# Kernel tuning notes

Hardware: AMD Instinct MI355X
Metric: run time of the kernel (lower is better)

The kernel has to match this reference:

```python
import jax, jax.numpy as jnp
import numpy as np

B, C, H, W = 16, 64, 64, 64
K_CLUST, KS, OUT, RANK, MLP = 16, 3, 64, 8, 32
F = C * KS * KS  # 576


def setup_inputs() -> dict:
    key = jax.random.key(0)
    ks = jax.random.split(key, 14)
    rn = lambda k, shp, s=0.05: (jax.random.normal(k, shp, jnp.float32) * s)
    return {
        "x": jax.random.normal(ks[0], (B, C, H, W), jnp.float32),
        "labels": jax.random.randint(ks[1], (B, H, W), 0, K_CLUST),
        "lr_w1": rn(ks[2], (F, MLP)), "lr_b1": rn(ks[3], (MLP,)),
        "lr_w2": rn(ks[4], (MLP, MLP)), "lr_b2": rn(ks[5], (MLP,)),
        "lr_w3": rn(ks[6], (MLP, RANK)), "lr_b3": rn(ks[7], (RANK,)),
        "base_kernels": rn(ks[8], (RANK, F, OUT), 0.1),
        "bw1": rn(ks[9], (F, MLP)), "bb1": rn(ks[10], (MLP,)),
        "bw2": rn(ks[11], (MLP, OUT)), "bb2": rn(ks[12], (OUT,)),
    }


def _extract_patches(x):
    # torch nn.Unfold(kernel=3, padding=1) layout: features ordered (C, kh, kw)
    b, c, h, w = x.shape
    xp = jnp.pad(x, ((0, 0), (0, 0), (1, 1), (1, 1)))
    p = jnp.stack([xp[:, :, i:i + h, j:j + w] for i in range(KS) for j in range(KS)], axis=2)  # [B,C,9,H,W]
    return p.reshape(b, c * KS * KS, h * w).transpose(0, 2, 1)  # [B, HW, F]


def reference(x, labels, lr_w1, lr_b1, lr_w2, lr_b2, lr_w3, lr_b3,
              base_kernels, bw1, bb1, bw2, bb2):
    b, c, h, w = x.shape
    patches = _extract_patches(x)                              # [B, HW, F]
    lab = labels.reshape(b, -1)                                # [B, HW]
    onehot = jax.nn.one_hot(lab, K_CLUST, dtype=patches.dtype) # [B, HW, K]
    counts = onehot.sum(axis=1)                                # [B, K]
    centers = jnp.einsum('bnk,bnf->bkf', onehot, patches) / (counts[:, :, None] + 1e-6)

    hdn = jax.nn.relu(centers @ lr_w1 + lr_b1)
    hdn = jax.nn.relu(hdn @ lr_w2 + lr_b2)
    lowrank = hdn @ lr_w3 + lr_b3                              # [B, K, R]
    bias = jax.nn.relu(centers @ bw1 + bb1) @ bw2 + bb2        # [B, K, O]

    kernels = jnp.einsum('bkr,rfo->bkfo', lowrank, base_kernels)   # [B, K, F, O]
    scores = jnp.einsum('bnf,bkfo->bnko', patches, kernels)        # [B, HW, K, O]
    out = jnp.einsum('bnko,bnk->bno', scores, onehot)
    out = out + jnp.einsum('bko,bnk->bno', bias, onehot)           # per-pixel cluster bias
    return out.reshape(b, h, w, OUT).transpose(0, 3, 1, 2)         # [B, O, H, W]
```

## Files before the change

kernel.cpp:

```cpp
#include <hip/hip_runtime.h>
#include <stdint.h>
#include <stddef.h>

#define NB   16
#define NC   64
#define NH   64
#define NW   64
#define KC   16
#define NOUT 64
#define NRANK 8
#define NMLP 32
#define NF   576
#define NPIX 4096
#define XH   66

typedef short s16x8 __attribute__((ext_vector_type(8)));
typedef short s16x4 __attribute__((ext_vector_type(4)));
typedef float f32x4 __attribute__((ext_vector_type(4)));

__device__ __forceinline__ unsigned short f2bf(float x) {
    union { float f; uint32_t u; } v; v.f = x;
    uint32_t r = v.u + 0x7FFFu + ((v.u >> 16) & 1u);
    return (unsigned short)(r >> 16);
}
__device__ __forceinline__ float bf2f(unsigned short u) {
    union { uint32_t u; float f; } v; v.u = ((uint32_t)u) << 16;
    return v.f;
}

extern "C" __global__ __launch_bounds__(256)
void k_prep_all(const float* __restrict__ x, const float* __restrict__ basek,
                unsigned short* __restrict__ xcl, unsigned short* __restrict__ basekF)
{
    __shared__ float tile[64 * 65];
    const int blk0 = blockIdx.x;
    const int tid = threadIdx.x;
    if (blk0 < XH * 16) {
        const int b = blk0 & 15, yy = blk0 >> 4;
        unsigned short* dst = xcl + ((size_t)(b * XH + yy) * XH) * 64;
        if (yy == 0 || yy == XH - 1) {
            for (int e = tid; e < XH * 64; e += 256) dst[e] = 0;
            return;
        }
        const int y = yy - 1;
        const float* src = x + (size_t)b * NC * (NH * NW) + y * NW;
        #pragma unroll
        for (int rr = 0; rr < 16; ++rr) {
            int c = rr * 4 + (tid >> 6);
            int xx = tid & 63;
            tile[c * 65 + xx] = src[(size_t)c * (NH * NW) + xx];
        }
        __syncthreads();
        for (int ee = tid; ee < 528; ee += 256) {
            int xx = ee >> 3;
            int c0 = (ee & 7) * 8;
            s16x8 v;
            #pragma unroll
            for (int j = 0; j < 8; ++j) {
                float f = (xx == 0 || xx == XH - 1) ? 0.f : tile[(c0 + j) * 65 + (xx - 1)];
                v[j] = (short)f2bf(f);
            }
            *reinterpret_cast<s16x8*>(dst + ee * 8) = v;
        }
    } else {
        const int blk = blk0 - XH * 16;
        const int ks = blk >> 2, wv = blk & 3;
        unsigned short outv[16];
        #pragma unroll
        for (int i = 0; i < 16; ++i) {
            int e = tid * 16 + i;
            int r = e >> 9;
            int lane = (e >> 3) & 63;
            int j = e & 7;
            int col = wv * 16 + (lane & 15);
            int fp = (lane >> 4) * 8 + ks * 32 + j;
            int tap = fp >> 6, c = fp & 63;
            outv[i] = f2bf(basek[((size_t)r * NF + c * 9 + tap) * NOUT + col]);
        }
        unsigned short* dst = basekF + (size_t)blk * 4096 + tid * 16;
        #pragma unroll
        for (int i = 0; i < 16; ++i) dst[i] = outv[i];
    }
}

extern "C" __global__ __launch_bounds__(1024)
void k_centers(const unsigned short* __restrict__ xcl, const int* __restrict__ labels,
               const float* __restrict__ lw1, const float* __restrict__ lb1,
               const float* __restrict__ lw2, const float* __restrict__ lb2,
               const float* __restrict__ lw3, const float* __restrict__ lb3,
               const float* __restrict__ bw1, const float* __restrict__ bb1,
               const float* __restrict__ bw2, const float* __restrict__ bb2,
               const unsigned short* __restrict__ basekF,
               unsigned short* __restrict__ lists, unsigned short* __restrict__ slotmap,
               int* __restrict__ counts, float* __restrict__ biasrows,
               unsigned short* __restrict__ wt)
{
    const int bk = blockIdx.x;
    const int b = bk & 15, k = bk >> 4;
    __shared__ unsigned short list[NPIX];
    __shared__ int wcnt[16];
    __shared__ float wsum[16 * 9 * 64];
    __shared__ float cbuf[NF];
    __shared__ float p1[8][NMLP], pb[8][NMLP];
    __shared__ float h1[NMLP], h2[NMLP], hb[NMLP], lrs[NRANK];
    const int tid = threadIdx.x;
    const int lane = tid & 63, wv = tid >> 6;
    const int* lab = labels + b * NPIX;

    int total = 0;
    #pragma unroll 1
    for (int base = 0; base < NPIX; base += 1024) {
        int n = base + tid;
        bool pred = (lab[n] == k);
        unsigned long long m = __ballot(pred);
        if (lane == 0) wcnt[wv] = __popcll(m);
        int pre = __popcll(m & ((1ull << lane) - 1ull));
        __syncthreads();
        int wbase = total;
        for (int i = 0; i < wv; ++i) wbase += wcnt[i];
        int nt = total;
        for (int i = 0; i < 16; ++i) nt += wcnt[i];
        if (pred) {
            int slot = wbase + pre;
            list[slot] = (unsigned short)n;
            slotmap[b * NPIX + n] = (unsigned short)slot;
        }
        total = nt;
        __syncthreads();
    }
    const int cnt = total;
    for (int i = tid; i < cnt; i += 1024) lists[bk * NPIX + i] = list[i];
    if (tid == 0) counts[bk] = cnt;
    __syncthreads();

    float s00 = 0.f, s01 = 0.f, s02 = 0.f,
          s10 = 0.f, s11 = 0.f, s12 = 0.f,
          s20 = 0.f, s21 = 0.f, s22 = 0.f;
    const unsigned short* xb = xcl + (size_t)b * (XH * XH * 64) + lane;
    #pragma unroll 2
    for (int i = wv; i < cnt; i += 16) {
        int n = list[i];
        const unsigned short* p0 = xb + (((n >> 6) * XH) + (n & 63)) * 64;
        s00 += bf2f(p0[0]);
        s01 += bf2f(p0[64]);
        s02 += bf2f(p0[128]);
        const unsigned short* prow1 = p0 + XH * 64;
        s10 += bf2f(prow1[0]);
        s11 += bf2f(prow1[64]);
        s12 += bf2f(prow1[128]);
        const unsigned short* prow2 = p0 + 2 * XH * 64;
        s20 += bf2f(prow2[0]);
        s21 += bf2f(prow2[64]);
        s22 += bf2f(prow2[128]);
    }
    {
        float* wrow = wsum + wv * 576 + lane;
        wrow[0 * 64] = s00; wrow[1 * 64] = s01; wrow[2 * 64] = s02;
        wrow[3 * 64] = s10; wrow[4 * 64] = s11; wrow[5 * 64] = s12;
        wrow[6 * 64] = s20; wrow[7 * 64] = s21; wrow[8 * 64] = s22;
    }
    __syncthreads();

    const float inv = 1.f / ((float)cnt + 1e-6f);
    if (tid < NF) {
        int tap = tid >> 6, c = tid & 63;
        float s = 0.f;
        #pragma unroll
        for (int w = 0; w < 16; ++w) s += wsum[w * 576 + tap * 64 + c];
        cbuf[c * 9 + tap] = s * inv;
    }
    __syncthreads();

    if (tid < 256) {
        const int j = tid & 31, ch = tid >> 5;
        float a1 = 0.f, a2 = 0.f;
        for (int i = 0; i < 72; ++i) {
            int f = ch * 72 + i;
            float cv = cbuf[f];
            a1 += cv * lw1[f * NMLP + j];
            a2 += cv * bw1[f * NMLP + j];
        }
        p1[ch][j] = a1; pb[ch][j] = a2;
    }
    __syncthreads();
    if (tid < NMLP) {
        float a = lb1[tid];
        for (int i = 0; i < 8; ++i) a += p1[i][tid];
        h1[tid] = fmaxf(a, 0.f);
    } else if (tid < 2 * NMLP) {
        int j = tid - NMLP;
        float a = bb1[j];
        for (int i = 0; i < 8; ++i) a += pb[i][j];
        hb[j] = fmaxf(a, 0.f);
    }
    __syncthreads();
    if (tid < NMLP) {
        float a = lb2[tid];
        for (int i = 0; i < NMLP; ++i) a += h1[i] * lw2[i * NMLP + tid];
        h2[tid] = fmaxf(a, 0.f);
    } else if (tid >= 64 && tid < 128) {
        int o = tid - 64;
        float a = bb2[o];
        for (int i = 0; i < NMLP; ++i) a += hb[i] * bw2[i * NOUT + o];
        biasrows[bk * NOUT + o] = a;
    }
    __syncthreads();
    if (tid < NRANK) {
        float a = lb3[tid];
        for (int i = 0; i < NMLP; ++i) a += h2[i] * lw3[i * NRANK + tid];
        lrs[tid] = a;
    }
    __syncthreads();

    float l8[NRANK];
    #pragma unroll
    for (int r = 0; r < NRANK; ++r) l8[r] = lrs[r];
    unsigned short* wtg = wt + (size_t)bk * (18 * 2048);
    #pragma unroll 2
    for (int q = 0; q < 5; ++q) {
        int m = q * 1024 + tid;
        if (m < 4608) {
            int ks = m >> 8, t = m & 255;
            const unsigned short* src = basekF
                + ((size_t)(ks * 4 + (t >> 6)) * 8) * 512 + (t & 63) * 8;
            float w[8] = {0.f, 0.f, 0.f, 0.f, 0.f, 0.f, 0.f, 0.f};
            #pragma unroll
            for (int r = 0; r < NRANK; ++r) {
                s16x8 bv = *reinterpret_cast<const s16x8*>(src + r * 512);
                #pragma unroll
                for (int j = 0; j < 8; ++j)
                    w[j] += l8[r] * bf2f((unsigned short)bv[j]);
            }
            s16x8 f;
            #pragma unroll
            for (int j = 0; j < 8; ++j) f[j] = (short)f2bf(w[j]);
            *reinterpret_cast<s16x8*>(wtg + ks * 2048 + t * 8) = f;
        }
    }
}

extern "C" __global__ __launch_bounds__(256)
void k_main(const unsigned short* __restrict__ xcl, const unsigned short* __restrict__ lists,
            const int* __restrict__ counts, const unsigned short* __restrict__ wt,
            const float* __restrict__ biasrows, unsigned short* __restrict__ outc)
{
    const int blk = blockIdx.x;
    const int bk = blk & 255, split = blk >> 8;
    const int b = bk & 15, k = bk >> 4;
    const int tid = threadIdx.x;
    const int lane = tid & 63, wv = tid >> 6;
    const int quad = lane >> 4, l16 = lane & 15;
    const int cnt = counts[bk];
    int prefix = 0;
    for (int kk = 0; kk < k; ++kk) prefix += counts[kk * 16 + b];

    __shared__ __align__(16) unsigned short albuf[32 * 584];
    __shared__ float biasl[NOUT];

    if (tid < NOUT) biasl[tid] = biasrows[bk * NOUT + tid];

    const int col = wv * 16 + l16;
    const unsigned short* wsrc = wt + (size_t)bk * (18 * 2048) + tid * 8;
    s16x8 bfr[18];
    #pragma unroll
    for (int ks = 0; ks < 18; ++ks)
        bfr[ks] = *reinterpret_cast<const s16x8*>(wsrc + ks * 2048);

    const unsigned short* xb = xcl + (size_t)b * (XH * XH * 64);
    const unsigned short* gl = lists + bk * NPIX;
    const int p = tid >> 3, part = tid & 7;
    const int ntile = (cnt + 31) >> 5;

    for (int t = split; t < ntile; t += 4) {
        int slot = (t << 5) + p;
        int n = (slot < cnt) ? (int)gl[slot] : 0;
        const unsigned short* xrow = xb + (((n >> 6) * XH) + (n & 63)) * 64 + part * 8;
        unsigned short* arow = albuf + p * 584 + part * 8;
        #pragma unroll
        for (int tap = 0; tap < 9; ++tap) {
            int dy = tap / 3, dx = tap - dy * 3;
            *reinterpret_cast<s16x8*>(arow + tap * 64) =
                *reinterpret_cast<const s16x8*>(xrow + (dy * XH + dx) * 64);
        }
        __syncthreads();

        f32x4 acc0 = {0.f, 0.f, 0.f, 0.f}, acc1 = {0.f, 0.f, 0.f, 0.f};
        const unsigned short* ar0 = albuf + l16 * 584 + quad * 8;
        const unsigned short* ar1 = ar0 + 16 * 584;
        #pragma unroll
        for (int ks = 0; ks < 18; ++ks) {
            s16x8 a0 = *reinterpret_cast<const s16x8*>(ar0 + ks * 32);
            s16x8 a1 = *reinterpret_cast<const s16x8*>(ar1 + ks * 32);
            acc0 = __builtin_amdgcn_mfma_f32_16x16x32_bf16(a0, bfr[ks], acc0, 0, 0, 0);
            acc1 = __builtin_amdgcn_mfma_f32_16x16x32_bf16(a1, bfr[ks], acc1, 0, 0, 0);
        }
        __syncthreads();

        float bb = biasl[col];
        unsigned short* ob = outc + ((size_t)b * NPIX + prefix) * 64;
        #pragma unroll
        for (int r = 0; r < 4; ++r) {
            int s0 = (t << 5) + quad * 4 + r;
            if (s0 < cnt) ob[(size_t)s0 * 64 + col] = f2bf(acc0[r] + bb);
            int s1 = s0 + 16;
            if (s1 < cnt) ob[(size_t)s1 * 64 + col] = f2bf(acc1[r] + bb);
        }
    }
}

extern "C" __global__ __launch_bounds__(256)
void k_scatter(const int* __restrict__ labels, const unsigned short* __restrict__ slotmap,
               const int* __restrict__ counts, const unsigned short* __restrict__ outc,
               float* __restrict__ out)
{
    const int blk = blockIdx.x;
    const int b = blk & 15, chunk = (blk >> 4) & 15, q = blk >> 8;
    const int tid = threadIdx.x;
    __shared__ int pref[KC];
    __shared__ int sptr[256];
    __shared__ unsigned short tt[256 * 20];
    if (tid < KC) {
        int s = 0;
        for (int kk = 0; kk < tid; ++kk) s += counts[kk * 16 + b];
        pref[tid] = s;
    }
    __syncthreads();
    const int n0 = chunk * 256;
    {
        int n = n0 + tid;
        sptr[tid] = pref[labels[b * NPIX + n]] + (int)slotmap[b * NPIX + n];
    }
    __syncthreads();
    #pragma unroll
    for (int e0 = 0; e0 < 2; ++e0) {
        int e = e0 * 256 + tid;
        int pix = e >> 1, part = e & 1;
        s16x8 vv = *reinterpret_cast<const s16x8*>(
            outc + ((size_t)b * NPIX + sptr[pix]) * 64 + q * 16 + part * 8);
        s16x4 lo = {vv[0], vv[1], vv[2], vv[3]};
        s16x4 hi = {vv[4], vv[5], vv[6], vv[7]};
        *reinterpret_cast<s16x4*>(tt + pix * 20 + part * 8) = lo;
        *reinterpret_cast<s16x4*>(tt + pix * 20 + part * 8 + 4) = hi;
    }
    __syncthreads();
    float* ob = out + ((size_t)(b * NOUT + q * 16)) * NPIX + n0;
    #pragma unroll
    for (int oo = 0; oo < 16; ++oo)
        ob[(size_t)oo * NPIX + tid] = bf2f(tt[tid * 20 + oo]);
}

extern "C" void kernel_launch(void* const* d_in, const int* in_sizes, int n_in,
                              void* d_out, int out_size, void* d_ws, size_t ws_size,
                              hipStream_t stream)
{
    const float* x      = (const float*)d_in[0];
    const int*   labels = (const int*)d_in[1];
    const float* lw1    = (const float*)d_in[2];
    const float* lb1    = (const float*)d_in[3];
    const float* lw2    = (const float*)d_in[4];
    const float* lb2    = (const float*)d_in[5];
    const float* lw3    = (const float*)d_in[6];
    const float* lb3    = (const float*)d_in[7];
    const float* basek  = (const float*)d_in[8];
    const float* bw1    = (const float*)d_in[9];
    const float* bb1    = (const float*)d_in[10];
    const float* bw2    = (const float*)d_in[11];
    const float* bb2    = (const float*)d_in[12];
    float* out = (float*)d_out;

    char* ws = (char*)d_ws;
    unsigned short* lists   = (unsigned short*)(ws);
    int*            counts  = (int*)(ws + 2097152);
    float*          biasrows= (float*)(ws + 2098176);
    unsigned short* basekF  = (unsigned short*)(ws + 2163712);
    unsigned short* slotmap = (unsigned short*)(ws + 2753536);
    unsigned short* xcl     = (unsigned short*)(ws + 2884608);
    unsigned short* outc    = (unsigned short*)(ws + 11805696);
    unsigned short* wt      = (unsigned short*)(ws + 20194304);

    k_prep_all<<<XH * 16 + 72, 256, 0, stream>>>(x, basek, xcl, basekF);
    k_centers<<<256, 1024, 0, stream>>>(xcl, labels, lw1, lb1, lw2, lb2, lw3, lb3,
                                        bw1, bb1, bw2, bb2, basekF,
                                        lists, slotmap, counts, biasrows, wt);
    k_main<<<1024, 256, 0, stream>>>(xcl, lists, counts, wt, biasrows, outc);
    k_scatter<<<1024, 256, 0, stream>>>(labels, slotmap, counts, outc, out);
}
```

Baseline: 141.4 us.

## Build per-cluster weights in LDS inside main GEMM kernel, waves own tiles

The low-rank kernel synthesis moves from k_centers into k_main. Each of 256 blocks of 1024 threads builds its cluster's bf16 weight matrix in LDS, which removes the global write and read-back of the per-cluster weights. The pixel-tile loop is restructured so each wave owns a whole 32-row tile and all 64 output columns. A operands are read straight from global memory and B fragments come from LDS, so the per-tile block barriers and A staging buffer are gone. The cost is fewer blocks than before (256 vs 1024), possible load imbalance between waves from uneven cluster sizes, and dynamic LDS of about 72KB.

New measurement: 176.4 us. +24.7%, slower.

```diff
diff --git a/kernel.cpp b/kernel.cpp
--- a/kernel.cpp
+++ b/kernel.cpp
@@ -90,10 +90,9 @@
                const float* __restrict__ lw3, const float* __restrict__ lb3,
                const float* __restrict__ bw1, const float* __restrict__ bb1,
                const float* __restrict__ bw2, const float* __restrict__ bb2,
-               const unsigned short* __restrict__ basekF,
                unsigned short* __restrict__ lists, unsigned short* __restrict__ slotmap,
                int* __restrict__ counts, float* __restrict__ biasrows,
-               unsigned short* __restrict__ wt)
+               float* __restrict__ lrsbuf)
 {
     const int bk = blockIdx.x;
     const int b = bk & 15, k = bk >> 4;
@@ -102,7 +101,7 @@
     __shared__ float wsum[16 * 9 * 64];
     __shared__ float cbuf[NF];
     __shared__ float p1[8][NMLP], pb[8][NMLP];
-    __shared__ float h1[NMLP], h2[NMLP], hb[NMLP], lrs[NRANK];
+    __shared__ float h1[NMLP], h2[NMLP], hb[NMLP];
     const int tid = threadIdx.x;
     const int lane = tid & 63, wv = tid >> 6;
     const int* lab = labels + b * NPIX;
@@ -208,44 +207,20 @@
     if (tid < NRANK) {
         float a = lb3[tid];
         for (int i = 0; i < NMLP; ++i) a += h2[i] * lw3[i * NRANK + tid];
-        lrs[tid] = a;
-    }
-    __syncthreads();
-
-    float l8[NRANK];
-    #pragma unroll
-    for (int r = 0; r < NRANK; ++r) l8[r] = lrs[r];
-    unsigned short* wtg = wt + (size_t)bk * (18 * 2048);
-    #pragma unroll 2
-    for (int q = 0; q < 5; ++q) {
-        int m = q * 1024 + tid;
-        if (m < 4608) {
-            int ks = m >> 8, t = m & 255;
-            const unsigned short* src = basekF
-                + ((size_t)(ks * 4 + (t >> 6)) * 8) * 512 + (t & 63) * 8;
-            float w[8] = {0.f, 0.f, 0.f, 0.f, 0.f, 0.f, 0.f, 0.f};
-            #pragma unroll
-            for (int r = 0; r < NRANK; ++r) {
-                s16x8 bv = *reinterpret_cast<const s16x8*>(src + r * 512);
-                #pragma unroll
-                for (int j = 0; j < 8; ++j)
-                    w[j] += l8[r] * bf2f((unsigned short)bv[j]);
-            }
-            s16x8 f;
-            #pragma unroll
-            for (int j = 0; j < 8; ++j) f[j] = (short)f2bf(w[j]);
-            *reinterpret_cast<s16x8*>(wtg + ks * 2048 + t * 8) = f;
-        }
-    }
-}
-
-extern "C" __global__ __launch_bounds__(256)
+        lrsbuf[bk * NRANK + tid] = a;
+    }
+}
+
+extern "C" __global__ __launch_bounds__(1024)
 void k_main(const unsigned short* __restrict__ xcl, const unsigned short* __restrict__ lists,
-            const int* __restrict__ counts, const unsigned short* __restrict__ wt,
-            const float* __restrict__ biasrows, unsigned short* __restrict__ outc)
-{
-    const int blk = blockIdx.x;
-    const int bk = blk & 255, split = blk >> 8;
+            const int* __restrict__ counts, const float* __restrict__ lrsbuf,
+            const unsigned short* __restrict__ basekF, const float* __restrict__ biasrows,
+            unsigned short* __restrict__ outc)
+{
+    extern __shared__ __align__(16) unsigned short Wl[];
+    float* biasl = (float*)(Wl + 18 * 2048);
+
+    const int bk = blockIdx.x;
     const int b = bk & 15, k = bk >> 4;
     const int tid = threadIdx.x;
     const int lane = tid & 63, wv = tid >> 6;
@@ -254,56 +229,83 @@
     int prefix = 0;
     for (int kk = 0; kk < k; ++kk) prefix += counts[kk * 16 + b];
 
-    __shared__ __align__(16) unsigned short albuf[32 * 584];
-    __shared__ float biasl[NOUT];
-
     if (tid < NOUT) biasl[tid] = biasrows[bk * NOUT + tid];
 
-    const int col = wv * 16 + l16;
-    const unsigned short* wsrc = wt + (size_t)bk * (18 * 2048) + tid * 8;
-    s16x8 bfr[18];
-    #pragma unroll
-    for (int ks = 0; ks < 18; ++ks)
-        bfr[ks] = *reinterpret_cast<const s16x8*>(wsrc + ks * 2048);
+    {
+        float l8[NRANK];
+        #pragma unroll
+        for (int r = 0; r < NRANK; ++r) l8[r] = lrsbuf[bk * NRANK + r];
+        #pragma unroll
+        for (int q = 0; q < 5; ++q) {
+            int m = q * 1024 + tid;
+            if (m < 4608) {
+                int ks = m >> 8, t = m & 255;
+                const unsigned short* src = basekF
+                    + ((size_t)(ks * 4 + (t >> 6)) * 8) * 512 + (t & 63) * 8;
+                float w[8] = {0.f, 0.f, 0.f, 0.f, 0.f, 0.f, 0.f, 0.f};
+                #pragma unroll
+                for (int r = 0; r < NRANK; ++r) {
+                    s16x8 bv = *reinterpret_cast<const s16x8*>(src + r * 512);
+                    #pragma unroll
+                    for (int j = 0; j < 8; ++j)
+                        w[j] += l8[r] * bf2f((unsigned short)bv[j]);
+                }
+                s16x8 f;
+                #pragma unroll
+                for (int j = 0; j < 8; ++j) f[j] = (short)f2bf(w[j]);
+                *reinterpret_cast<s16x8*>(Wl + m * 8) = f;
+            }
+        }
+    }
+    __syncthreads();
 
     const unsigned short* xb = xcl + (size_t)b * (XH * XH * 64);
     const unsigned short* gl = lists + bk * NPIX;
-    const int p = tid >> 3, part = tid & 7;
     const int ntile = (cnt + 31) >> 5;
 
-    for (int t = split; t < ntile; t += 4) {
-        int slot = (t << 5) + p;
-        int n = (slot < cnt) ? (int)gl[slot] : 0;
-        const unsigned short* xrow = xb + (((n >> 6) * XH) + (n & 63)) * 64 + part * 8;
-        unsigned short* arow = albuf + p * 584 + part * 8;
-        #pragma unroll
-        for (int tap = 0; tap < 9; ++tap) {
-            int dy = tap / 3, dx = tap - dy * 3;
-            *reinterpret_cast<s16x8*>(arow + tap * 64) =
-                *reinterpret_cast<const s16x8*>(xrow + (dy * XH + dx) * 64);
-        }
-        __syncthreads();
-
-        f32x4 acc0 = {0.f, 0.f, 0.f, 0.f}, acc1 = {0.f, 0.f, 0.f, 0.f};
-        const unsigned short* ar0 = albuf + l16 * 584 + quad * 8;
-        const unsigned short* ar1 = ar0 + 16 * 584;
+    for (int t = wv; t < ntile; t += 16) {
+        int s0 = (t << 5) + l16;
+        int s1 = s0 + 16;
+        int n0 = (s0 < cnt) ? (int)gl[s0] : 0;
+        int n1 = (s1 < cnt) ? (int)gl[s1] : 0;
+        const unsigned short* pA = xb + (((n0 >> 6) * XH) + (n0 & 63)) * 64 + quad * 8;
+        const unsigned short* pB = xb + (((n1 >> 6) * XH) + (n1 & 63)) * 64 + quad * 8;
+
+        f32x4 acc[4][2];
+        #pragma unroll
+        for (int cg = 0; cg < 4; ++cg) {
+            acc[cg][0] = (f32x4){0.f, 0.f, 0.f, 0.f};
+            acc[cg][1] = (f32x4){0.f, 0.f, 0.f, 0.f};
+        }
+
         #pragma unroll
         for (int ks = 0; ks < 18; ++ks) {
-            s16x8 a0 = *reinterpret_cast<const s16x8*>(ar0 + ks * 32);
-            s16x8 a1 = *reinterpret_cast<const s16x8*>(ar1 + ks * 32);
-            acc0 = __builtin_amdgcn_mfma_f32_16x16x32_bf16(a0, bfr[ks], acc0, 0, 0, 0);
-            acc1 = __builtin_amdgcn_mfma_f32_16x16x32_bf16(a1, bfr[ks], acc1, 0, 0, 0);
-        }
-        __syncthreads();
-
-        float bb = biasl[col];
+            const int tap = ks >> 1;
+            const int dy = tap / 3, dx = tap - dy * 3;
+            const int off = (dy * XH + dx) * 64 + (ks & 1) * 32;
+            s16x8 a0 = *reinterpret_cast<const s16x8*>(pA + off);
+            s16x8 a1 = *reinterpret_cast<const s16x8*>(pB + off);
+            #pragma unroll
+            for (int cg = 0; cg < 4; ++cg) {
+                s16x8 bfrag = *reinterpret_cast<const s16x8*>(
+                    Wl + ks * 2048 + (cg * 64 + lane) * 8);
+                acc[cg][0] = __builtin_amdgcn_mfma_f32_16x16x32_bf16(a0, bfrag, acc[cg][0], 0, 0, 0);
+                acc[cg][1] = __builtin_amdgcn_mfma_f32_16x16x32_bf16(a1, bfrag, acc[cg][1], 0, 0, 0);
+            }
+        }
+
         unsigned short* ob = outc + ((size_t)b * NPIX + prefix) * 64;
         #pragma unroll
-        for (int r = 0; r < 4; ++r) {
-            int s0 = (t << 5) + quad * 4 + r;
-            if (s0 < cnt) ob[(size_t)s0 * 64 + col] = f2bf(acc0[r] + bb);
-            int s1 = s0 + 16;
-            if (s1 < cnt) ob[(size_t)s1 * 64 + col] = f2bf(acc1[r] + bb);
+        for (int cg = 0; cg < 4; ++cg) {
+            const int col = cg * 16 + l16;
+            const float bb = biasl[col];
+            #pragma unroll
+            for (int r = 0; r < 4; ++r) {
+                int r0 = (t << 5) + quad * 4 + r;
+                if (r0 < cnt) ob[(size_t)r0 * 64 + col] = f2bf(acc[cg][0][r] + bb);
+                int r1 = r0 + 16;
+                if (r1 < cnt) ob[(size_t)r1 * 64 + col] = f2bf(acc[cg][1][r] + bb);
+            }
         }
     }
 }
@@ -376,12 +378,13 @@
     unsigned short* slotmap = (unsigned short*)(ws + 2753536);
     unsigned short* xcl     = (unsigned short*)(ws + 2884608);
     unsigned short* outc    = (unsigned short*)(ws + 11805696);
-    unsigned short* wt      = (unsigned short*)(ws + 20194304);
+    float*          lrsbuf  = (float*)(ws + 20194304);
 
     k_prep_all<<<XH * 16 + 72, 256, 0, stream>>>(x, basek, xcl, basekF);
     k_centers<<<256, 1024, 0, stream>>>(xcl, labels, lw1, lb1, lw2, lb2, lw3, lb3,
-                                        bw1, bb1, bw2, bb2, basekF,
-                                        lists, slotmap, counts, biasrows, wt);
-    k_main<<<1024, 256, 0, stream>>>(xcl, lists, counts, wt, biasrows, outc);
+                                        bw1, bb1, bw2, bb2,
+                                        lists, slotmap, counts, biasrows, lrsbuf);
+    k_main<<<256, 1024, 18 * 2048 * 2 + NOUT * 4, stream>>>(
+        xcl, lists, counts, lrsbuf, basekF, biasrows, outc);
     k_scatter<<<1024, 256, 0, stream>>>(labels, slotmap, counts, outc, out);
 }
```

## Compute cluster patch sums by scattering each input pixel with atomics

Applied to the files above, without the earlier changes.

The per-cluster center sums move out of the gather loop in k_centers into a new k_sums kernel. Each pixel value is read once and atomically added into shared-memory per-cluster accumulators for every 3x3 tap whose neighbouring label it touches. The block partials are then atomically added into a global csums buffer, which is zeroed by extra blocks in the prep kernel. This replaces the scattered, latency-bound gather of padded patches in k_centers, at the cost of one extra kernel launch, shared and global atomic contention, and a csums buffer that aliases the outc workspace.

After: 328.1 us. 132% more time.

```diff
diff --git a/kernel.cpp b/kernel.cpp
--- a/kernel.cpp
+++ b/kernel.cpp
@@ -30,7 +30,8 @@
 
 extern "C" __global__ __launch_bounds__(256)
 void k_prep_all(const float* __restrict__ x, const float* __restrict__ basek,
-                unsigned short* __restrict__ xcl, unsigned short* __restrict__ basekF)
+                unsigned short* __restrict__ xcl, unsigned short* __restrict__ basekF,
+                float* __restrict__ csums)
 {
     __shared__ float tile[64 * 65];
     const int blk0 = blockIdx.x;
@@ -62,7 +63,7 @@
             }
             *reinterpret_cast<s16x8*>(dst + ee * 8) = v;
         }
-    } else {
+    } else if (blk0 < XH * 16 + 72) {
         const int blk = blk0 - XH * 16;
         const int ks = blk >> 2, wv = blk & 3;
         unsigned short outv[16];
@@ -80,31 +81,86 @@
         unsigned short* dst = basekF + (size_t)blk * 4096 + tid * 16;
         #pragma unroll
         for (int i = 0; i < 16; ++i) dst[i] = outv[i];
+    } else {
+        const int idx = (blk0 - (XH * 16 + 72)) * 256 + tid;
+        for (int e = idx; e < 256 * NF; e += 2048) csums[e] = 0.f;
     }
 }
 
 extern "C" __global__ __launch_bounds__(1024)
-void k_centers(const unsigned short* __restrict__ xcl, const int* __restrict__ labels,
-               const float* __restrict__ lw1, const float* __restrict__ lb1,
-               const float* __restrict__ lw2, const float* __restrict__ lb2,
-               const float* __restrict__ lw3, const float* __restrict__ lb3,
-               const float* __restrict__ bw1, const float* __restrict__ bb1,
-               const float* __restrict__ bw2, const float* __restrict__ bb2,
-               const unsigned short* __restrict__ basekF,
-               unsigned short* __restrict__ lists, unsigned short* __restrict__ slotmap,
-               int* __restrict__ counts, float* __restrict__ biasrows,
-               unsigned short* __restrict__ wt)
+void k_sums(const unsigned short* __restrict__ xcl, const int* __restrict__ labels,
+            float* __restrict__ csums)
+{
+    __shared__ float sums[KC * NF];
+    __shared__ short labL[6 * 64];
+    const int tid = threadIdx.x;
+    const int lane = tid & 63, wv = tid >> 6;
+    const int b = blockIdx.x & 15, band = blockIdx.x >> 4;
+
+    for (int e = tid; e < KC * NF; e += 1024) sums[e] = 0.f;
+    if (tid < 384) {
+        int rr = tid >> 6, gx = tid & 63;
+        int gy = band * 4 - 1 + rr;
+        labL[tid] = (gy >= 0 && gy < 64) ? (short)labels[b * NPIX + gy * 64 + gx]
+                                         : (short)0;
+    }
+    __syncthreads();
+
+    const int yy = 1 + band * 4 + (wv & 3);
+    const int x0 = 1 + (wv >> 2) * 16;
+    const unsigned short* xrow = xcl + (((size_t)(b * XH + yy)) * XH + x0) * 64 + lane;
+    const int lbase = band * 4 - 1;
+
+    for (int i = 0; i < 16; ++i) {
+        int xx = x0 + i;
+        float v = bf2f(xrow[i * 64]);
+        #pragma unroll
+        for (int dy = 0; dy < 3; ++dy) {
+            int qy = yy - dy;
+            if ((unsigned)qy >= 64u) continue;
+            const short* lrow = labL + (qy - lbase) * 64;
+            #pragma unroll
+            for (int dx = 0; dx < 3; ++dx) {
+                int qx = xx - dx;
+                if ((unsigned)qx >= 64u) continue;
+                int k = (int)lrow[qx];
+                __hip_atomic_fetch_add(&sums[k * NF + (dy * 3 + dx) * 64 + lane], v,
+                                       __ATOMIC_RELAXED, __HIP_MEMORY_SCOPE_WORKGROUP);
+            }
+        }
+    }
+    __syncthreads();
+
+    for (int e = tid; e < KC * NF; e += 1024) {
+        int k = e / NF;
+        int r = e - k * NF;
+        __hip_atomic_fetch_add(&csums[((size_t)(k * 16 + b)) * NF + r], sums[e],
+                               __ATOMIC_RELAXED, __HIP_MEMORY_SCOPE_AGENT);
+    }
+}
+
+extern "C" __global__ __launch_bounds__(1024)
+void k_centers2(const int* __restrict__ labels,
+                const float* __restrict__ lw1, const float* __restrict__ lb1,
+                const float* __restrict__ lw2, const float* __restrict__ lb2,
+                const float* __restrict__ lw3, const float* __restrict__ lb3,
+                const float* __restrict__ bw1, const float* __restrict__ bb1,
+                const float* __restrict__ bw2, const float* __restrict__ bb2,
+                const unsigned short* __restrict__ basekF, const float* __restrict__ csums,
+                unsigned short* __restrict__ lists, unsigned short* __restrict__ slotmap,
+                int* __restrict__ counts, float* __restrict__ biasrows,
+                unsigned short* __restrict__ wt)
 {
     const int bk = blockIdx.x;
-    const int b = bk & 15, k = bk >> 4;
+    const int b = bk & 15;
     __shared__ unsigned short list[NPIX];
     __shared__ int wcnt[16];
-    __shared__ float wsum[16 * 9 * 64];
     __shared__ float cbuf[NF];
     __shared__ float p1[8][NMLP], pb[8][NMLP];
     __shared__ float h1[NMLP], h2[NMLP], hb[NMLP], lrs[NRANK];
     const int tid = threadIdx.x;
     const int lane = tid & 63, wv = tid >> 6;
+    const int k = bk >> 4;
     const int* lab = labels + b * NPIX;
 
     int total = 0;
@@ -131,43 +187,11 @@
     const int cnt = total;
     for (int i = tid; i < cnt; i += 1024) lists[bk * NPIX + i] = list[i];
     if (tid == 0) counts[bk] = cnt;
-    __syncthreads();
-
-    float s00 = 0.f, s01 = 0.f, s02 = 0.f,
-          s10 = 0.f, s11 = 0.f, s12 = 0.f,
-          s20 = 0.f, s21 = 0.f, s22 = 0.f;
-    const unsigned short* xb = xcl + (size_t)b * (XH * XH * 64) + lane;
-    #pragma unroll 2
-    for (int i = wv; i < cnt; i += 16) {
-        int n = list[i];
-        const unsigned short* p0 = xb + (((n >> 6) * XH) + (n & 63)) * 64;
-        s00 += bf2f(p0[0]);
-        s01 += bf2f(p0[64]);
-        s02 += bf2f(p0[128]);
-        const unsigned short* prow1 = p0 + XH * 64;
-        s10 += bf2f(prow1[0]);
-        s11 += bf2f(prow1[64]);
-        s12 += bf2f(prow1[128]);
-        const unsigned short* prow2 = p0 + 2 * XH * 64;
-        s20 += bf2f(prow2[0]);
-        s21 += bf2f(prow2[64]);
-        s22 += bf2f(prow2[128]);
-    }
-    {
-        float* wrow = wsum + wv * 576 + lane;
-        wrow[0 * 64] = s00; wrow[1 * 64] = s01; wrow[2 * 64] = s02;
-        wrow[3 * 64] = s10; wrow[4 * 64] = s11; wrow[5 * 64] = s12;
-        wrow[6 * 64] = s20; wrow[7 * 64] = s21; wrow[8 * 64] = s22;
-    }
-    __syncthreads();
 
     const float inv = 1.f / ((float)cnt + 1e-6f);
     if (tid < NF) {
         int tap = tid >> 6, c = tid & 63;
-        float s = 0.f;
-        #pragma unroll
-        for (int w = 0; w < 16; ++w) s += wsum[w * 576 + tap * 64 + c];
-        cbuf[c * 9 + tap] = s * inv;
+        cbuf[c * 9 + tap] = csums[(size_t)bk * NF + tid] * inv;
     }
     __syncthreads();
 
@@ -376,12 +400,14 @@
     unsigned short* slotmap = (unsigned short*)(ws + 2753536);
     unsigned short* xcl     = (unsigned short*)(ws + 2884608);
     unsigned short* outc    = (unsigned short*)(ws + 11805696);
+    float*          csums   = (float*)(ws + 11805696);
     unsigned short* wt      = (unsigned short*)(ws + 20194304);
 
-    k_prep_all<<<XH * 16 + 72, 256, 0, stream>>>(x, basek, xcl, basekF);
-    k_centers<<<256, 1024, 0, stream>>>(xcl, labels, lw1, lb1, lw2, lb2, lw3, lb3,
-                                        bw1, bb1, bw2, bb2, basekF,
-                                        lists, slotmap, counts, biasrows, wt);
+    k_prep_all<<<XH * 16 + 72 + 8, 256, 0, stream>>>(x, basek, xcl, basekF, csums);
+    k_sums<<<256, 1024, 0, stream>>>(xcl, labels, csums);
+    k_centers2<<<256, 1024, 0, stream>>>(labels, lw1, lb1, lw2, lb2, lw3, lb3,
+                                         bw1, bb1, bw2, bb2, basekF, csums,
+                                         lists, slotmap, counts, biasrows, wt);
     k_main<<<1024, 256, 0, stream>>>(xcl, lists, counts, wt, biasrows, outc);
     k_scatter<<<1024, 256, 0, stream>>>(labels, slotmap, counts, outc, out);
 }
```

## Fuse prep, centers and main GEMM into one persistent kernel with grid barriers

Applied to the files above, without the earlier changes.

Three kernels (input repack, cluster centers/MLP/weight synthesis, per-cluster MFMA GEMM) are merged into one persistent 256-block, 1024-thread kernel. Phases are separated by atomic-counter grid barriers whose counters live in the first bytes of the output buffer, zeroed with a memset, and the GEMM tiles are spread over four 256-thread subgroups within a block. The aim is to remove kernel launch gaps and inter-kernel drain/fill costs. The trade-off is reliance on all 256 blocks being co-resident, a large dynamic shared allocation, and one block per CU for the GEMM phase, which cuts occupancy.

Measured after the change: 446.6 us. 216% more time.

```diff
diff --git a/kernel.cpp b/kernel.cpp
--- a/kernel.cpp
+++ b/kernel.cpp
@@ -13,6 +13,7 @@
 #define NF   576
 #define NPIX 4096
 #define XH   66
+#define NBLK 256
 
 typedef short s16x8 __attribute__((ext_vector_type(8)));
 typedef short s16x4 __attribute__((ext_vector_type(4)));
@@ -28,282 +29,313 @@
     return v.f;
 }
 
-extern "C" __global__ __launch_bounds__(256)
-void k_prep_all(const float* __restrict__ x, const float* __restrict__ basek,
-                unsigned short* __restrict__ xcl, unsigned short* __restrict__ basekF)
+__device__ __forceinline__ void gbar(int* c) {
+    __threadfence();
+    __syncthreads();
+    if (threadIdx.x == 0) {
+        __hip_atomic_fetch_add(c, 1, __ATOMIC_ACQ_REL, __HIP_MEMORY_SCOPE_AGENT);
+        while (__hip_atomic_load(c, __ATOMIC_ACQUIRE, __HIP_MEMORY_SCOPE_AGENT) < NBLK)
+            __builtin_amdgcn_s_sleep(2);
+    }
+    __syncthreads();
+    __threadfence();
+}
+
+extern "C" __global__ __launch_bounds__(1024, 1)
+void k_fused(const float* __restrict__ x, const int* __restrict__ labels,
+             const float* __restrict__ lw1, const float* __restrict__ lb1,
+             const float* __restrict__ lw2, const float* __restrict__ lb2,
+             const float* __restrict__ lw3, const float* __restrict__ lb3,
+             const float* __restrict__ basek,
+             const float* __restrict__ bw1, const float* __restrict__ bb1,
+             const float* __restrict__ bw2, const float* __restrict__ bb2,
+             unsigned short* __restrict__ xcl, unsigned short* __restrict__ basekF,
+             unsigned short* __restrict__ lists, unsigned short* __restrict__ slotmap,
+             int* __restrict__ counts, float* __restrict__ biasrows,
+             unsigned short* __restrict__ wt, unsigned short* __restrict__ outc,
+             int* __restrict__ bars)
 {
-    __shared__ float tile[64 * 65];
-    const int blk0 = blockIdx.x;
+    extern __shared__ __align__(16) char smem[];
     const int tid = threadIdx.x;
-    if (blk0 < XH * 16) {
-        const int b = blk0 & 15, yy = blk0 >> 4;
-        unsigned short* dst = xcl + ((size_t)(b * XH + yy) * XH) * 64;
-        if (yy == 0 || yy == XH - 1) {
-            for (int e = tid; e < XH * 64; e += 256) dst[e] = 0;
-            return;
-        }
-        const int y = yy - 1;
-        const float* src = x + (size_t)b * NC * (NH * NW) + y * NW;
+    const int st = tid & 255, sg = tid >> 8;
+    const int lane = tid & 63;
+
+    {
+        float* tileF = (float*)(smem + sg * 16640);
+        #pragma unroll 1
+        for (int pass = 0; pass < 2; ++pass) {
+            const int u = pass * 1024 + sg * 256 + blockIdx.x;
+            const bool valid = (u < XH * 16);
+            const int b = u & 15, yy = u >> 4;
+            const bool interior = valid && (yy > 0) && (yy < XH - 1);
+            if (interior) {
+                const float* src = x + (size_t)b * NC * (NH * NW) + (yy - 1) * NW;
+                #pragma unroll
+                for (int rr = 0; rr < 16; ++rr) {
+                    int c = rr * 4 + (st >> 6);
+                    int xx = st & 63;
+                    tileF[c * 65 + xx] = src[(size_t)c * (NH * NW) + xx];
+                }
+            }
+            __syncthreads();
+            if (valid) {
+                unsigned short* dst = xcl + ((size_t)(b * XH + yy) * XH) * 64;
+                if (!interior) {
+                    for (int e = st; e < XH * 64; e += 256) dst[e] = 0;
+                } else {
+                    for (int ee = st; ee < 528; ee += 256) {
+                        int xx = ee >> 3;
+                        int c0 = (ee & 7) * 8;
+                        s16x8 v;
+                        #pragma unroll
+                        for (int j = 0; j < 8; ++j) {
+                            float f = (xx == 0 || xx == XH - 1)
+                                          ? 0.f : tileF[(c0 + j) * 65 + (xx - 1)];
+                            v[j] = (short)f2bf(f);
+                        }
+                        *reinterpret_cast<s16x8*>(dst + ee * 8) = v;
+                    }
+                }
+            }
+            __syncthreads();
+        }
+        const int u2 = blockIdx.x * 4 + sg;
+        if (u2 < 72) {
+            const int ks = u2 >> 2, wvq = u2 & 3;
+            unsigned short outv[16];
+            #pragma unroll
+            for (int i = 0; i < 16; ++i) {
+                int e = st * 16 + i;
+                int r = e >> 9;
+                int lane8 = (e >> 3) & 63;
+                int j = e & 7;
+                int col = wvq * 16 + (lane8 & 15);
+                int fp = (lane8 >> 4) * 8 + ks * 32 + j;
+                int tap = fp >> 6, c = fp & 63;
+                outv[i] = f2bf(basek[((size_t)r * NF + c * 9 + tap) * NOUT + col]);
+            }
+            unsigned short* dst = basekF + (size_t)u2 * 4096 + st * 16;
+            #pragma unroll
+            for (int i = 0; i < 16; ++i) dst[i] = outv[i];
+        }
+    }
+    gbar(&bars[0]);
+
+    {
+        unsigned short* list = (unsigned short*)smem;
+        int*   wcnt = (int*)(smem + 8192);
+        float* wsum = (float*)(smem + 8256);
+        float* cbuf = (float*)(smem + 45120);
+        float* p1   = (float*)(smem + 47424);
+        float* pb   = (float*)(smem + 48448);
+        float* h1   = (float*)(smem + 49472);
+        float* h2   = (float*)(smem + 49600);
+        float* hb   = (float*)(smem + 49728);
+        float* lrs  = (float*)(smem + 49856);
+        const int bk = blockIdx.x;
+        const int b = bk & 15, k = bk >> 4;
+        const int wv = tid >> 6;
+        const int* lab = labels + b * NPIX;
+
+        int total = 0;
+        #pragma unroll 1
+        for (int base = 0; base < NPIX; base += 1024) {
+            int n = base + tid;
+            bool pred = (lab[n] == k);
+            unsigned long long m = __ballot(pred);
+            if (lane == 0) wcnt[wv] = __popcll(m);
+            int pre = __popcll(m & ((1ull << lane) - 1ull));
+            __syncthreads();
+            int wbase = total;
+            for (int i = 0; i < wv; ++i) wbase += wcnt[i];
+            int nt = total;
+            for (int i = 0; i < 16; ++i) nt += wcnt[i];
+            if (pred) {
+                int slot = wbase + pre;
+                list[slot] = (unsigned short)n;
+                slotmap[b * NPIX + n] = (unsigned short)slot;
+            }
+            total = nt;
+            __syncthreads();
+        }
+        const int cnt = total;
+        for (int i = tid; i < cnt; i += 1024) lists[bk * NPIX + i] = list[i];
+        if (tid == 0) counts[bk] = cnt;
+        __syncthreads();
+
+        float s00 = 0.f, s01 = 0.f, s02 = 0.f,
+              s10 = 0.f, s11 = 0.f, s12 = 0.f,
+              s20 = 0.f, s21 = 0.f, s22 = 0.f;
+        const unsigned short* xb = xcl + (size_t)b * (XH * XH * 64) + lane;
+        #pragma unroll 2
+        for (int i = wv; i < cnt; i += 16) {
+            int n = list[i];
+            const unsigned short* p0 = xb + (((n >> 6) * XH) + (n & 63)) * 64;
+            s00 += bf2f(p0[0]);
+            s01 += bf2f(p0[64]);
+            s02 += bf2f(p0[128]);
+            const unsigned short* prow1 = p0 + XH * 64;
+            s10 += bf2f(prow1[0]);
+            s11 += bf2f(prow1[64]);
+            s12 += bf2f(prow1[128]);
+            const unsigned short* prow2 = p0 + 2 * XH * 64;
+            s20 += bf2f(prow2[0]);
+            s21 += bf2f(prow2[64]);
+            s22 += bf2f(prow2[128]);
+        }
+        {
+            float* wrow = wsum + wv * 576 + lane;
+            wrow[0 * 64] = s00; wrow[1 * 64] = s01; wrow[2 * 64] = s02;
+            wrow[3 * 64] = s10; wrow[4 * 64] = s11; wrow[5 * 64] = s12;
+            wrow[6 * 64] = s20; wrow[7 * 64] = s21; wrow[8 * 64] = s22;
+        }
+        __syncthreads();
+
+        const float inv = 1.f / ((float)cnt + 1e-6f);
+        if (tid < NF) {
+            int tap = tid >> 6, c = tid & 63;
+            float s = 0.f;
+            #pragma unroll
+            for (int w = 0; w < 16; ++w) s += wsum[w * 576 + tap * 64 + c];
+            cbuf[c * 9 + tap] = s * inv;
+        }
+        __syncthreads();
+
+        if (tid < 256) {
+            const int j = tid & 31, ch = tid >> 5;
+            float a1 = 0.f, a2 = 0.f;
+            for (int i = 0; i < 72; ++i) {
+                int f = ch * 72 + i;
+                float cv = cbuf[f];
+                a1 += cv * lw1[f * NMLP + j];
+                a2 += cv * bw1[f * NMLP + j];
+            }
+            p1[ch * NMLP + j] = a1; pb[ch * NMLP + j] = a2;
+        }
+        __syncthreads();
+        if (tid < NMLP) {
+            float a = lb1[tid];
+            for (int i = 0; i < 8; ++i) a += p1[i * NMLP + tid];
+            h1[tid] = fmaxf(a, 0.f);
+        } else if (tid < 2 * NMLP) {
+            int j = tid - NMLP;
+            float a = bb1[j];
+            for (int i = 0; i < 8; ++i) a += pb[i * NMLP + j];
+            hb[j] = fmaxf(a, 0.f);
+        }
+        __syncthreads();
+        if (tid < NMLP) {
+            float a = lb2[tid];
+            for (int i = 0; i < NMLP; ++i) a += h1[i] * lw2[i * NMLP + tid];
+            h2[tid] = fmaxf(a, 0.f);
+        } else if (tid >= 64 && tid < 128) {
+            int o = tid - 64;
+            float a = bb2[o];
+            for (int i = 0; i < NMLP; ++i) a += hb[i] * bw2[i * NOUT + o];
+            biasrows[bk * NOUT + o] = a;
+        }
+        __syncthreads();
+        if (tid < NRANK) {
+            float a = lb3[tid];
+            for (int i = 0; i < NMLP; ++i) a += h2[i] * lw3[i * NRANK + tid];
+            lrs[tid] = a;
+        }
+        __syncthreads();
+
+        float l8[NRANK];
         #pragma unroll
-        for (int rr = 0; rr < 16; ++rr) {
-            int c = rr * 4 + (tid >> 6);
-            int xx = tid & 63;
-            tile[c * 65 + xx] = src[(size_t)c * (NH * NW) + xx];
-        }
-        __syncthreads();
-        for (int ee = tid; ee < 528; ee += 256) {
-            int xx = ee >> 3;
-            int c0 = (ee & 7) * 8;
-            s16x8 v;
-            #pragma unroll
-            for (int j = 0; j < 8; ++j) {
-                float f = (xx == 0 || xx == XH - 1) ? 0.f : tile[(c0 + j) * 65 + (xx - 1)];
-                v[j] = (short)f2bf(f);
-            }
-            *reinterpret_cast<s16x8*>(dst + ee * 8) = v;
-        }
-    } else {
-        const int blk = blk0 - XH * 16;
-        const int ks = blk >> 2, wv = blk & 3;
-        unsigned short outv[16];
+        for (int r = 0; r < NRANK; ++r) l8[r] = lrs[r];
+        unsigned short* wtg = wt + (size_t)bk * (18 * 2048);
+        #pragma unroll 2
+        for (int q = 0; q < 5; ++q) {
+            int m = q * 1024 + tid;
+            if (m < 4608) {
+                int ks = m >> 8, t = m & 255;
+                const unsigned short* src = basekF
+                    + ((size_t)(ks * 4 + (t >> 6)) * 8) * 512 + (t & 63) * 8;
+                float w[8] = {0.f, 0.f, 0.f, 0.f, 0.f, 0.f, 0.f, 0.f};
+                #pragma unroll
+                for (int r = 0; r < NRANK; ++r) {
+                    s16x8 bv = *reinterpret_cast<const s16x8*>(src + r * 512);
+                    #pragma unroll
+                    for (int j = 0; j < 8; ++j)
+                        w[j] += l8[r] * bf2f((unsigned short)bv[j]);
+                }
+                s16x8 f;
+                #pragma unroll
+                for (int j = 0; j < 8; ++j) f[j] = (short)f2bf(w[j]);
+                *reinterpret_cast<s16x8*>(wtg + ks * 2048 + t * 8) = f;
+            }
+        }
+    }
+    gbar(&bars[1]);
+
+    {
+        const int bk = blockIdx.x;
+        const int b = bk & 15, k = bk >> 4;
+        const int wv4 = (tid >> 6) & 3;
+        const int quad = lane >> 4, l16 = lane & 15;
+        const int cnt = counts[bk];
+        int prefix = 0;
+        for (int kk = 0; kk < k; ++kk) prefix += counts[kk * 16 + b];
+
+        unsigned short* albuf = (unsigned short*)(smem + sg * 37376);
+        float* biasl = (float*)(smem + 4 * 37376);
+        if (tid < NOUT) biasl[tid] = biasrows[bk * NOUT + tid];
+
+        const int col = wv4 * 16 + l16;
+        const unsigned short* wsrc = wt + (size_t)bk * (18 * 2048) + st * 8;
+        s16x8 bfr[18];
         #pragma unroll
-        for (int i = 0; i < 16; ++i) {
-            int e = tid * 16 + i;
-            int r = e >> 9;
-            int lane = (e >> 3) & 63;
-            int j = e & 7;
-            int col = wv * 16 + (lane & 15);
-            int fp = (lane >> 4) * 8 + ks * 32 + j;
-            int tap = fp >> 6, c = fp & 63;
-            outv[i] = f2bf(basek[((size_t)r * NF + c * 9 + tap) * NOUT + col]);
-        }
-        unsigned short* dst = basekF + (size_t)blk * 4096 + tid * 16;
-        #pragma unroll
-        for (int i = 0; i < 16; ++i) dst[i] = outv[i];
-    }
-}
-
-extern "C" __global__ __launch_bounds__(1024)
-void k_centers(const unsigned short* __restrict__ xcl, const int* __restrict__ labels,
-               const float* __restrict__ lw1, const float* __restrict__ lb1,
-               const float* __restrict__ lw2, const float* __restrict__ lb2,
-               const float* __restrict__ lw3, const float* __restrict__ lb3,
-               const float* __restrict__ bw1, const float* __restrict__ bb1,
-               const float* __restrict__ bw2, const float* __restrict__ bb2,
-               const unsigned short* __restrict__ basekF,
-               unsigned short* __restrict__ lists, unsigned short* __restrict__ slotmap,
-               int* __restrict__ counts, float* __restrict__ biasrows,
-               unsigned short* __restrict__ wt)
-{
-    const int bk = blockIdx.x;
-    const int b = bk & 15, k = bk >> 4;
-    __shared__ unsigned short list[NPIX];
-    __shared__ int wcnt[16];
-    __shared__ float wsum[16 * 9 * 64];
-    __shared__ float cbuf[NF];
-    __shared__ float p1[8][NMLP], pb[8][NMLP];
-    __shared__ float h1[NMLP], h2[NMLP], hb[NMLP], lrs[NRANK];
-    const int tid = threadIdx.x;
-    const int lane = tid & 63, wv = tid >> 6;
-    const int* lab = labels + b * NPIX;
-
-    int total = 0;
-    #pragma unroll 1
-    for (int base = 0; base < NPIX; base += 1024) {
-        int n = base + tid;
-        bool pred = (lab[n] == k);
-        unsigned long long m = __ballot(pred);
-        if (lane == 0) wcnt[wv] = __popcll(m);
-        int pre = __popcll(m & ((1ull << lane) - 1ull));
-        __syncthreads();
-        int wbase = total;
-        for (int i = 0; i < wv; ++i) wbase += wcnt[i];
-        int nt = total;
-        for (int i = 0; i < 16; ++i) nt += wcnt[i];
-        if (pred) {
-            int slot = wbase + pre;
-            list[slot] = (unsigned short)n;
-            slotmap[b * NPIX + n] = (unsigned short)slot;
-        }
-        total = nt;
-        __syncthreads();
-    }
-    const int cnt = total;
-    for (int i = tid; i < cnt; i += 1024) lists[bk * NPIX + i] = list[i];
-    if (tid == 0) counts[bk] = cnt;
-    __syncthreads();
-
-    float s00 = 0.f, s01 = 0.f, s02 = 0.f,
-          s10 = 0.f, s11 = 0.f, s12 = 0.f,
-          s20 = 0.f, s21 = 0.f, s22 = 0.f;
-    const unsigned short* xb = xcl + (size_t)b * (XH * XH * 64) + lane;
-    #pragma unroll 2
-    for (int i = wv; i < cnt; i += 16) {
-        int n = list[i];
-        const unsigned short* p0 = xb + (((n >> 6) * XH) + (n & 63)) * 64;
-        s00 += bf2f(p0[0]);
-        s01 += bf2f(p0[64]);
-        s02 += bf2f(p0[128]);
-        const unsigned short* prow1 = p0 + XH * 64;
-        s10 += bf2f(prow1[0]);
-        s11 += bf2f(prow1[64]);
-        s12 += bf2f(prow1[128]);
-        const unsigned short* prow2 = p0 + 2 * XH * 64;
-        s20 += bf2f(prow2[0]);
-        s21 += bf2f(prow2[64]);
-        s22 += bf2f(prow2[128]);
-    }
-    {
-        float* wrow = wsum + wv * 576 + lane;
-        wrow[0 * 64] = s00; wrow[1 * 64] = s01; wrow[2 * 64] = s02;
-        wrow[3 * 64] = s10; wrow[4 * 64] = s11; wrow[5 * 64] = s12;
-        wrow[6 * 64] = s20; wrow[7 * 64] = s21; wrow[8 * 64] = s22;
-    }
-    __syncthreads();
-
-    const float inv = 1.f / ((float)cnt + 1e-6f);
-    if (tid < NF) {
-        int tap = tid >> 6, c = tid & 63;
-        float s = 0.f;
-        #pragma unroll
-        for (int w = 0; w < 16; ++w) s += wsum[w * 576 + tap * 64 + c];
-        cbuf[c * 9 + tap] = s * inv;
-    }
-    __syncthreads();
-
-    if (tid < 256) {
-        const int j = tid & 31, ch = tid >> 5;
-        float a1 = 0.f, a2 = 0.f;
-        for (int i = 0; i < 72; ++i) {
-            int f = ch * 72 + i;
-            float cv = cbuf[f];
-            a1 += cv * lw1[f * NMLP + j];
-            a2 += cv * bw1[f * NMLP + j];
-        }
-        p1[ch][j] = a1; pb[ch][j] = a2;
-    }
-    __syncthreads();
-    if (tid < NMLP) {
-        float a = lb1[tid];
-        for (int i = 0; i < 8; ++i) a += p1[i][tid];
-        h1[tid] = fmaxf(a, 0.f);
-    } else if (tid < 2 * NMLP) {
-        int j = tid - NMLP;
-        float a = bb1[j];
-        for (int i = 0; i < 8; ++i) a += pb[i][j];
-        hb[j] = fmaxf(a, 0.f);
-    }
-    __syncthreads();
-    if (tid < NMLP) {
-        float a = lb2[tid];
-        for (int i = 0; i < NMLP; ++i) a += h1[i] * lw2[i * NMLP + tid];
-        h2[tid] = fmaxf(a, 0.f);
-    } else if (tid >= 64 && tid < 128) {
-        int o = tid - 64;
-        float a = bb2[o];
-        for (int i = 0; i < NMLP; ++i) a += hb[i] * bw2[i * NOUT + o];
-        biasrows[bk * NOUT + o] = a;
-    }
-    __syncthreads();
-    if (tid < NRANK) {
-        float a = lb3[tid];
-        for (int i = 0; i < NMLP; ++i) a += h2[i] * lw3[i * NRANK + tid];
-        lrs[tid] = a;
-    }
-    __syncthreads();
-
-    float l8[NRANK];
-    #pragma unroll
-    for (int r = 0; r < NRANK; ++r) l8[r] = lrs[r];
-    unsigned short* wtg = wt + (size_t)bk * (18 * 2048);
-    #pragma unroll 2
-    for (int q = 0; q < 5; ++q) {
-        int m = q * 1024 + tid;
-        if (m < 4608) {
-            int ks = m >> 8, t = m & 255;
-            const unsigned short* src = basekF
-                + ((size_t)(ks * 4 + (t >> 6)) * 8) * 512 + (t & 63) * 8;
-            float w[8] = {0.f, 0.f, 0.f, 0.f, 0.f, 0.f, 0.f, 0.f};
-            #pragma unroll
-            for (int r = 0; r < NRANK; ++r) {
-                s16x8 bv = *reinterpret_cast<const s16x8*>(src + r * 512);
-                #pragma unroll
-                for (int j = 0; j < 8; ++j)
-                    w[j] += l8[r] * bf2f((unsigned short)bv[j]);
-            }
-            s16x8 f;
-            #pragma unroll
-            for (int j = 0; j < 8; ++j) f[j] = (short)f2bf(w[j]);
-            *reinterpret_cast<s16x8*>(wtg + ks * 2048 + t * 8) = f;
-        }
-    }
-}
-
-extern "C" __global__ __launch_bounds__(256)
-void k_main(const unsigned short* __restrict__ xcl, const unsigned short* __restrict__ lists,
-            const int* __restrict__ counts, const unsigned short* __restrict__ wt,
-            const float* __restrict__ biasrows, unsigned short* __restrict__ outc)
-{
-    const int blk = blockIdx.x;
-    const int bk = blk & 255, split = blk >> 8;
-    const int b = bk & 15, k = bk >> 4;
-    const int tid = threadIdx.x;
-    const int lane = tid & 63, wv = tid >> 6;
-    const int quad = lane >> 4, l16 = lane & 15;
-    const int cnt = counts[bk];
-    int prefix = 0;
-    for (int kk = 0; kk < k; ++kk) prefix += counts[kk * 16 + b];
-
-    __shared__ __align__(16) unsigned short albuf[32 * 584];
-    __shared__ float biasl[NOUT];
-
-    if (tid < NOUT) biasl[tid] = biasrows[bk * NOUT + tid];
-
-    const int col = wv * 16 + l16;
-    const unsigned short* wsrc = wt + (size_t)bk * (18 * 2048) + tid * 8;
-    s16x8 bfr[18];
-    #pragma unroll
-    for (int ks = 0; ks < 18; ++ks)
-        bfr[ks] = *reinterpret_cast<const s16x8*>(wsrc + ks * 2048);
-
-    const unsigned short* xb = xcl + (size_t)b * (XH * XH * 64);
-    const unsigned short* gl = lists + bk * NPIX;
-    const int p = tid >> 3, part = tid & 7;
-    const int ntile = (cnt + 31) >> 5;
-
-    for (int t = split; t < ntile; t += 4) {
-        int slot = (t << 5) + p;
-        int n = (slot < cnt) ? (int)gl[slot] : 0;
-        const unsigned short* xrow = xb + (((n >> 6) * XH) + (n & 63)) * 64 + part * 8;
-        unsigned short* arow = albuf + p * 584 + part * 8;
-        #pragma unroll
-        for (int tap = 0; tap < 9; ++tap) {
-            int dy = tap / 3, dx = tap - dy * 3;
-            *reinterpret_cast<s16x8*>(arow + tap * 64) =
-                *reinterpret_cast<const s16x8*>(xrow + (dy * XH + dx) * 64);
-        }
-        __syncthreads();
-
-        f32x4 acc0 = {0.f, 0.f, 0.f, 0.f}, acc1 = {0.f, 0.f, 0.f, 0.f};
-        const unsigned short* ar0 = albuf + l16 * 584 + quad * 8;
-        const unsigned short* ar1 = ar0 + 16 * 584;
-        #pragma unroll
-        for (int ks = 0; ks < 18; ++ks) {
-            s16x8 a0 = *reinterpret_cast<const s16x8*>(ar0 + ks * 32);
-            s16x8 a1 = *reinterpret_cast<const s16x8*>(ar1 + ks * 32);
-            acc0 = __builtin_amdgcn_mfma_f32_16x16x32_bf16(a0, bfr[ks], acc0, 0, 0, 0);
-            acc1 = __builtin_amdgcn_mfma_f32_16x16x32_bf16(a1, bfr[ks], acc1, 0, 0, 0);
-        }
-        __syncthreads();
-
-        float bb = biasl[col];
+        for (int ks = 0; ks < 18; ++ks)
+            bfr[ks] = *reinterpret_cast<const s16x8*>(wsrc + ks * 2048);
+
+        const unsigned short* xb = xcl + (size_t)b * (XH * XH * 64);
+        const unsigned short* gl = lists + bk * NPIX;
+        const int p = st >> 3, part = st & 7;
+        const int ntile = (cnt + 31) >> 5;
+        const int niter = (ntile + 3) >> 2;
         unsigned short* ob = outc + ((size_t)b * NPIX + prefix) * 64;
-        #pragma unroll
-        for (int r = 0; r < 4; ++r) {
-            int s0 = (t << 5) + quad * 4 + r;
-            if (s0 < cnt) ob[(size_t)s0 * 64 + col] = f2bf(acc0[r] + bb);
-            int s1 = s0 + 16;
-            if (s1 < cnt) ob[(size_t)s1 * 64 + col] = f2bf(acc1[r] + bb);
+
+        #pragma unroll 1
+        for (int it = 0; it < niter; ++it) {
+            const int t = it * 4 + sg;
+            const bool live = (t < ntile);
+            if (live) {
+                int slot = (t << 5) + p;
+                int n = (slot < cnt) ? (int)gl[slot] : 0;
+                const unsigned short* xrow =
+                    xb + (((n >> 6) * XH) + (n & 63)) * 64 + part * 8;
+                unsigned short* arow = albuf + p * 584 + part * 8;
+                #pragma unroll
+                for (int tap = 0; tap < 9; ++tap) {
+                    int dy = tap / 3, dx = tap - dy * 3;
+                    *reinterpret_cast<s16x8*>(arow + tap * 64) =
+                        *reinterpret_cast<const s16x8*>(xrow + (dy * XH + dx) * 64);
+                }
+            }
+            __syncthreads();
+            if (live) {
+                f32x4 acc0 = {0.f, 0.f, 0.f, 0.f}, acc1 = {0.f, 0.f, 0.f, 0.f};
+                const unsigned short* ar0 = albuf + l16 * 584 + quad * 8;
+                const unsigned short* ar1 = ar0 + 16 * 584;
+                #pragma unroll
+                for (int ks = 0; ks < 18; ++ks) {
+                    s16x8 a0 = *reinterpret_cast<const s16x8*>(ar0 + ks * 32);
+                    s16x8 a1 = *reinterpret_cast<const s16x8*>(ar1 + ks * 32);
+                    acc0 = __builtin_amdgcn_mfma_f32_16x16x32_bf16(a0, bfr[ks], acc0, 0, 0, 0);
+                    acc1 = __builtin_amdgcn_mfma_f32_16x16x32_bf16(a1, bfr[ks], acc1, 0, 0, 0);
+                }
+                float bb = biasl[col];
+                #pragma unroll
+                for (int r = 0; r < 4; ++r) {
+                    int s0 = (t << 5) + quad * 4 + r;
+                    if (s0 < cnt) ob[(size_t)s0 * 64 + col] = f2bf(acc0[r] + bb);
+                    int s1 = s0 + 16;
+                    if (s1 < cnt) ob[(size_t)s1 * 64 + col] = f2bf(acc1[r] + bb);
+                }
+            }
+            __syncthreads();
         }
     }
 }
@@ -377,11 +409,12 @@
     unsigned short* xcl     = (unsigned short*)(ws + 2884608);
     unsigned short* outc    = (unsigned short*)(ws + 11805696);
     unsigned short* wt      = (unsigned short*)(ws + 20194304);
-
-    k_prep_all<<<XH * 16 + 72, 256, 0, stream>>>(x, basek, xcl, basekF);
-    k_centers<<<256, 1024, 0, stream>>>(xcl, labels, lw1, lb1, lw2, lb2, lw3, lb3,
-                                        bw1, bb1, bw2, bb2, basekF,
-                                        lists, slotmap, counts, biasrows, wt);
-    k_main<<<1024, 256, 0, stream>>>(xcl, lists, counts, wt, biasrows, outc);
+    int*            bars    = (int*)out;
+
+    hipMemsetAsync(out, 0, 8, stream);
+    k_fused<<<NBLK, 1024, 149760, stream>>>(x, labels, lw1, lb1, lw2, lb2, lw3, lb3,
+                                            basek, bw1, bb1, bw2, bb2,
+                                            xcl, basekF, lists, slotmap, counts,
+                                            biasrows, wt, outc, bars);
     k_scatter<<<1024, 256, 0, stream>>>(labels, slotmap, counts, outc, out);
 }
```
